# Optimization experiments

Hardware: AMD Instinct MI355X
Metric: run time of the kernel (lower is better)

Reference implementation:

```python
import jax, jax.numpy as jnp
import numpy as np
from jax import lax

# Fixed-point format: Q*.8 (8 fractional bits), as used by HGRNFixed8bit's
# to_fixed/from_fixed round-trip. We simulate it in float via round(x*256)/256.
FRAC = 256.0
EPS = 1e-5
B, T, D = 4, 2048, 2048  # batch, seq_len, hidden_size; input_dim = D (expand_ratio=1)


def to_fixed(x):
    return jnp.round(x * FRAC) / FRAC


def to_ternary(w):
    # BitNet-style ternarization: sign(w/mean|w|), zeroed where |w_norm| < 0.5
    scale = jnp.mean(jnp.abs(w))
    wn = w / (scale + 1e-5)
    t = jnp.sign(wn)
    return jnp.where(jnp.abs(wn) < 0.5, 0.0, t).astype(jnp.float32)


def per_channel_scale(w):
    # compute_scale: mean |w| over dim 0, stored in fixed point
    return to_fixed(jnp.mean(jnp.abs(w), axis=0))


def setup_inputs() -> dict:
    key = jax.random.key(0)
    ks = jax.random.split(key, 6)
    hidden_states = jax.random.normal(ks[0], (B, T, D), dtype=jnp.float32)
    # float master weights, then quantize exactly as quantize_weights() does
    w_i_f = jax.random.normal(ks[1], (D, D), dtype=jnp.float32) * 0.02  # i_proj.weight.T
    w_f_f = jax.random.normal(ks[2], (D, D), dtype=jnp.float32) * 0.02  # f_proj.weight.T
    w_g_f = jax.random.normal(ks[3], (D, D), dtype=jnp.float32) * 0.02  # g_proj.weight.T
    w_o_f = jax.random.normal(ks[4], (D, D), dtype=jnp.float32) * 0.02  # o_proj.weight [D_out, D_in]
    g_norm_w = jnp.ones((D,), dtype=jnp.float32)  # g_norm (RMSNorm-swish-gate) weight
    return {
        "hidden_states": hidden_states,
        "w_i": to_ternary(w_i_f), "w_f": to_ternary(w_f_f),
        "w_g": to_ternary(w_g_f), "w_o": to_ternary(w_o_f),
        "s_i": per_channel_scale(w_i_f), "s_f": per_channel_scale(w_f_f),
        "s_g": per_channel_scale(w_g_f), "s_o": per_channel_scale(w_o_f),
        "g_norm_w": g_norm_w,
    }


def reference(hidden_states, w_i, w_f, w_g, w_o, s_i, s_f, s_g, s_o, g_norm_w):
    # Quantize activations to 8-bit fixed point (to_fixed)
    x = to_fixed(hidden_states)                       # [B,T,D]
    # Ternary dequant-matmuls with per-channel scales
    i = jnp.einsum('btd,de->bte', x, w_i) * s_i       # input branch
    f = jax.nn.sigmoid(jnp.einsum('btd,de->bte', x, w_f) * s_f)  # forget gate
    g = jnp.einsum('btd,de->bte', x, w_g) * s_g       # output gate
    i = (1.0 - f) * i                                 # HGRN input gating
    # Gated linear recurrence h_t = f_t * h_{t-1} + i_t via associative scan
    def combine(a, b):
        af, ai = a
        bf, bi = b
        return (af * bf, ai * bf + bi)
    _, h = lax.associative_scan(combine, (f, i), axis=1)  # [B,T,E]
    # FusedRMSNormSwishGate: rmsnorm(h) * weight * swish(g)
    rms = h * lax.rsqrt(jnp.mean(h * h, axis=-1, keepdims=True) + EPS)
    o = rms * g_norm_w * (g * jax.nn.sigmoid(g))
    # Output ternary matmul (o_proj, weight untransposed -> use w_o.T),
    # per-input-channel scale, then from_fixed round-trip of the fixed output
    out = to_fixed(jnp.einsum('bte,oe->bto', o * s_o, w_o))  # [B,T,D]
    return out
```

## Files before the change

### kernel.cpp

```cpp
#include <hip/hip_runtime.h>
#include <hip/hip_bf16.h>
#include <stdint.h>
#include <math.h>


#define BATCH 4
#define SEQ   2048
#define DIM   2048
#define MROWS (BATCH*SEQ)
#define TCH   64
#define NCH   (SEQ/TCH)

#define GBM 256
#define GBN 128
#define GBK 64
#define GNT (DIM/GBK)
#define ASZ (GBM*GBK)
#define BSZ (GBN*GBK)
#define BUFSZ (ASZ+BSZ)

typedef unsigned short u16;
typedef __attribute__((ext_vector_type(8))) short short8;
typedef __attribute__((ext_vector_type(4))) float f32x4;

static __device__ __forceinline__ u16 f2bf_rne(float x) {
  uint32_t u = __float_as_uint(x);
  u += 0x7FFFu + ((u >> 16) & 1u);
  return (u16)(u >> 16);
}
static __device__ __forceinline__ float bf2f(u16 h) {
  return __uint_as_float(((uint32_t)h) << 16);
}

static __device__ __forceinline__ void gl2lds16(const void* g, void* l) {
  __builtin_amdgcn_global_load_lds((const __attribute__((address_space(1))) void*)g,
                                   (__attribute__((address_space(3))) void*)l,
                                   16, 0, 0);
}

__global__ __launch_bounds__(256) void diag_ws(float* __restrict__ out, float val) {
  size_t i = ((size_t)blockIdx.x * 256 + threadIdx.x) * 8;
#pragma unroll
  for (int j = 0; j < 8; j++) out[i + j] = val;
}

__global__ __launch_bounds__(256) void prep_x(const float* __restrict__ x,
                                              u16* __restrict__ XB) {
  size_t i = ((size_t)blockIdx.x * 256 + threadIdx.x) * 4;
  float4 v = *(const float4*)(x + i);
  float q[4] = {v.x, v.y, v.z, v.w};
  u16 hh[4];
#pragma unroll
  for (int j = 0; j < 4; j++) {
    float xq = rintf(q[j] * 256.0f) * 0.00390625f;
    hh[j] = f2bf_rne(xq);
  }
  *(uint2*)(XB + i) = make_uint2((uint32_t)hh[0] | ((uint32_t)hh[1] << 16),
                                 (uint32_t)hh[2] | ((uint32_t)hh[3] << 16));
}

__global__ void prep_wT(const float* __restrict__ w_i, const float* __restrict__ w_f,
                        const float* __restrict__ w_g, u16* __restrict__ WT) {
  __shared__ u16 tile[32][33];
  const int g = blockIdx.z;
  const float* __restrict__ w = (g == 0) ? w_i : (g == 1) ? w_f : w_g;
  u16* __restrict__ outp = WT + (size_t)g * DIM * DIM;
  const int d0 = blockIdx.x * 32;
  const int e0 = blockIdx.y * 32;
  const int tx = threadIdx.x;
  const int ty = threadIdx.y;
  for (int ii = ty; ii < 32; ii += 8)
    tile[ii][tx] = f2bf_rne(w[(size_t)(d0 + ii) * DIM + e0 + tx]);
  __syncthreads();
  for (int ii = ty; ii < 32; ii += 8)
    outp[(size_t)(e0 + ii) * DIM + d0 + tx] = tile[tx][ii];
}

__global__ __launch_bounds__(256) void prep_wo(const float* __restrict__ w, u16* __restrict__ WB) {
  size_t i = ((size_t)blockIdx.x * 256 + threadIdx.x) * 4;
  float4 v = *(const float4*)(w + i);
  *(uint2*)(WB + i) = make_uint2((uint32_t)f2bf_rne(v.x) | ((uint32_t)f2bf_rne(v.y) << 16),
                                 (uint32_t)f2bf_rne(v.z) | ((uint32_t)f2bf_rne(v.w) << 16));
}

static __device__ __forceinline__ void stage_A(const u16* ga, u16* buf, int tid) {
#pragma unroll
  for (int j = 0; j < 4; j++)
    gl2lds16(ga + (size_t)j * (64 * DIM), buf + (size_t)(tid + j * 512) * 8);
}
static __device__ __forceinline__ void stage_B(const u16* gb, u16* buf, int tid) {
#pragma unroll
  for (int j = 0; j < 2; j++)
    gl2lds16(gb + (size_t)j * (64 * DIM), buf + ASZ + (size_t)(tid + j * 512) * 8);
}

static __device__ __forceinline__ void kloop(const u16* __restrict__ Ag,
                                             const u16* __restrict__ Bg,
                                             u16* lds, f32x4 (&acc)[4][4]) {
  const int tid = threadIdx.x;
  const int lane16 = tid & 15;
  const int quad = (tid & 63) >> 4;
  const int wid = tid >> 6;
  const int waveM = wid >> 1;
  const int waveN = wid & 1;
  const int rowA = tid >> 3;
  const int cc8 = ((tid & 7) ^ (rowA & 7)) * 8;
  const u16* ga = Ag + (size_t)rowA * DIM + cc8;
  const u16* gb = Bg + (size_t)rowA * DIM + cc8;
  const int colx = (lane16 & 7) * 8;
  const int arow = (waveM * 64 + lane16) * GBK;
  const int brow = (waveN * 64 + lane16) * GBK;

  stage_A(ga, lds, tid);
  stage_B(gb, lds, tid);
  stage_A(ga + GBK, lds + BUFSZ, tid);
  stage_B(gb + GBK, lds + BUFSZ, tid);
  asm volatile("s_waitcnt vmcnt(6)" ::: "memory");
  __builtin_amdgcn_s_barrier();

  int sl = 0, st = 2;
#pragma unroll 1
  for (int t = 0; t < GNT; ++t) {
    const u16* A = lds + sl * BUFSZ;
    const u16* B = A + ASZ;
    u16* SB = lds + st * BUFSZ;
    const bool pf = (t + 2 < GNT);
    {
      short8 af[4], bf[4];
      const int c0 = (quad * 8) ^ colx;
#pragma unroll
      for (int mi = 0; mi < 4; mi++)
        af[mi] = *(const short8*)(A + arow + mi * (16 * GBK) + c0);
#pragma unroll
      for (int ni = 0; ni < 4; ni++)
        bf[ni] = *(const short8*)(B + brow + ni * (16 * GBK) + c0);
      if (pf) stage_A(ga + (size_t)(t + 2) * GBK, SB, tid);
      __builtin_amdgcn_s_barrier();
      __builtin_amdgcn_s_setprio(1);
#pragma unroll
      for (int mi = 0; mi < 4; mi++)
#pragma unroll
        for (int ni = 0; ni < 4; ni++)
          acc[mi][ni] = __builtin_amdgcn_mfma_f32_16x16x32_bf16(af[mi], bf[ni], acc[mi][ni], 0, 0, 0);
      __builtin_amdgcn_s_setprio(0);
      __builtin_amdgcn_s_barrier();
    }
    {
      short8 af[4], bf[4];
      const int c1 = (32 + quad * 8) ^ colx;
#pragma unroll
      for (int mi = 0; mi < 4; mi++)
        af[mi] = *(const short8*)(A + arow + mi * (16 * GBK) + c1);
#pragma unroll
      for (int ni = 0; ni < 4; ni++)
        bf[ni] = *(const short8*)(B + brow + ni * (16 * GBK) + c1);
      if (pf) stage_B(gb + (size_t)(t + 2) * GBK, SB, tid);
      __builtin_amdgcn_s_barrier();
      __builtin_amdgcn_s_setprio(1);
#pragma unroll
      for (int mi = 0; mi < 4; mi++)
#pragma unroll
        for (int ni = 0; ni < 4; ni++)
          acc[mi][ni] = __builtin_amdgcn_mfma_f32_16x16x32_bf16(af[mi], bf[ni], acc[mi][ni], 0, 0, 0);
      __builtin_amdgcn_s_setprio(0);
      __builtin_amdgcn_s_barrier();
    }
    if (pf) {
      asm volatile("s_waitcnt vmcnt(6)" ::: "memory");
    } else if (t + 1 < GNT) {
      asm volatile("s_waitcnt vmcnt(0)" ::: "memory");
    }
    __builtin_amdgcn_s_barrier();
    sl = (sl == 2) ? 0 : sl + 1;
    st = (st == 2) ? 0 : st + 1;
  }
}

__global__ __launch_bounds__(512, 2) void gemm_gates8(
    const u16* __restrict__ XB, const u16* __restrict__ WT,
    const float* __restrict__ s_i, const float* __restrict__ s_f, const float* __restrict__ s_g,
    const float* __restrict__ gnw, const float* __restrict__ s_o,
    u16* __restrict__ Ib, u16* __restrict__ Fb, u16* __restrict__ Gb) {
  __shared__ __align__(16) u16 lds[3 * BUFSZ];
  const int bid = blockIdx.x;
  const int i = (bid & 7) * 192 + (bid >> 3);
  const int gate = i >> 9;
  const int r = i & 511;
  const int m0 = (r >> 4) * GBM;
  const int n0 = (r & 15) * GBN;

  const u16* Ag = XB + (size_t)m0 * DIM;
  const u16* Bg = WT + (size_t)gate * DIM * DIM + (size_t)n0 * DIM;

  f32x4 acc[4][4];
#pragma unroll
  for (int a = 0; a < 4; a++)
#pragma unroll
    for (int b = 0; b < 4; b++) acc[a][b] = {0.f, 0.f, 0.f, 0.f};

  kloop(Ag, Bg, lds, acc);

  __syncthreads();
  const int tid = threadIdx.x;
  const int lane16 = tid & 15;
  const int quad = (tid & 63) >> 4;
  const int wid = tid >> 6;
  const int waveM = wid >> 1;
  const int waveN = wid & 1;
  const float* __restrict__ sc = (gate == 0) ? s_i : (gate == 1) ? s_f : s_g;
  u16* T = lds;
#pragma unroll
  for (int ni = 0; ni < 4; ni++) {
    const int n = n0 + waveN * 64 + ni * 16 + lane16;
    const float scale = sc[n];
    const float post = (gate == 2) ? gnw[n] * s_o[n] : 0.f;
    const int tcol = waveN * 64 + ni * 16 + lane16;
#pragma unroll
    for (int mi = 0; mi < 4; mi++) {
      const int lrow = waveM * 64 + mi * 16 + quad * 4;
#pragma unroll
      for (int r2 = 0; r2 < 4; r2++) {
        float v = acc[mi][ni][r2] * scale;
        if (gate == 1) v = 1.0f / (1.0f + expf(-v));
        if (gate == 2) v = v / (1.0f + expf(-v)) * post;
        T[(lrow + r2) * 136 + tcol] = f2bf_rne(v);
      }
    }
  }
  __syncthreads();
  u16* __restrict__ Out = (gate == 0) ? Ib : (gate == 1) ? Fb : Gb;
#pragma unroll
  for (int j = 0; j < 8; j++) {
    const int id = tid + j * 512;
    const int row = id >> 4;
    const int c16 = id & 15;
    uint4 v = *(const uint4*)(T + row * 136 + c16 * 8);
    *(uint4*)(Out + (size_t)(m0 + row) * DIM + n0 + c16 * 8) = v;
  }
}

__global__ __launch_bounds__(512, 2) void gemm_out8(const u16* __restrict__ OS,
                                                    const u16* __restrict__ WOB,
                                                    float* __restrict__ out) {
  __shared__ __align__(16) u16 lds[3 * BUFSZ];
  const int bid = blockIdx.x;
  const int i = (bid & 7) * 64 + (bid >> 3);
  const int m0 = (i >> 4) * GBM;
  const int n0 = (i & 15) * GBN;

  const u16* Ag = OS + (size_t)m0 * DIM;
  const u16* Bg = WOB + (size_t)n0 * DIM;

  f32x4 acc[4][4];
#pragma unroll
  for (int a = 0; a < 4; a++)
#pragma unroll
    for (int b = 0; b < 4; b++) acc[a][b] = {0.f, 0.f, 0.f, 0.f};

  kloop(Ag, Bg, lds, acc);

  __syncthreads();
  const int tid = threadIdx.x;
  const int lane16 = tid & 15;
  const int quad = (tid & 63) >> 4;
  const int wid = tid >> 6;
  const int waveM = wid >> 1;
  const int waveN = wid & 1;
  float* T = (float*)lds;
#pragma unroll
  for (int ni = 0; ni < 4; ni++) {
    const int tcol = waveN * 64 + ni * 16 + lane16;
#pragma unroll
    for (int mi = 0; mi < 4; mi++) {
      const int lrow = waveM * 64 + mi * 16 + quad * 4;
#pragma unroll
      for (int r2 = 0; r2 < 4; r2++)
        T[(lrow + r2) * 132 + tcol] = rintf(acc[mi][ni][r2] * 256.0f) * 0.00390625f;
    }
  }
  __syncthreads();
#pragma unroll
  for (int j = 0; j < 16; j++) {
    const int id = tid + j * 512;
    const int row = id >> 5;
    const int c4 = id & 31;
    float4 v = *(const float4*)(T + row * 132 + c4 * 4);
    *(float4*)(out + (size_t)(m0 + row) * DIM + n0 + c4 * 4) = v;
  }
}

__global__ __launch_bounds__(256) void scan_phase1(const u16* __restrict__ Fb,
                                                   const u16* __restrict__ Ib,
                                                   float* __restrict__ Pc,
                                                   float* __restrict__ Sc) {
  const int e0 = (blockIdx.x * 256 + threadIdx.x) * 2;
  const int c = blockIdx.y;
  const int b = blockIdx.z;
  const size_t base = ((size_t)b * SEQ + (size_t)c * TCH) * DIM + e0;
  float P0 = 1.f, S0 = 0.f, P1 = 1.f, S1 = 0.f;
  for (int t = 0; t < TCH; t++) {
    const uint32_t fp = *(const uint32_t*)(Fb + base + (size_t)t * DIM);
    const uint32_t ip = *(const uint32_t*)(Ib + base + (size_t)t * DIM);
    const float f0 = bf2f((u16)fp), f1 = bf2f((u16)(fp >> 16));
    const float i0 = bf2f((u16)ip), i1 = bf2f((u16)(ip >> 16));
    S0 = S0 * f0 + (1.f - f0) * i0;  P0 *= f0;
    S1 = S1 * f1 + (1.f - f1) * i1;  P1 *= f1;
  }
  const size_t ci = ((size_t)b * NCH + c) * DIM + e0;
  *(float2*)(Pc + ci) = make_float2(P0, P1);
  *(float2*)(Sc + ci) = make_float2(S0, S1);
}

__global__ __launch_bounds__(256) void scan_phase2(const u16* __restrict__ Fb,
                                                   const u16* __restrict__ Ib,
                                                   const float* __restrict__ Pc,
                                                   const float* __restrict__ Sc,
                                                   u16* __restrict__ Hb) {
  const int e0 = (blockIdx.x * 256 + threadIdx.x) * 2;
  const int c = blockIdx.y;
  const int b = blockIdx.z;
  float h0 = 0.f, h1 = 0.f;
  for (int cc = 0; cc < c; cc++) {
    const size_t ci = ((size_t)b * NCH + cc) * DIM + e0;
    const float2 p = *(const float2*)(Pc + ci);
    const float2 s = *(const float2*)(Sc + ci);
    h0 = s.x + p.x * h0;
    h1 = s.y + p.y * h1;
  }
  const size_t base = ((size_t)b * SEQ + (size_t)c * TCH) * DIM + e0;
  for (int t = 0; t < TCH; t++) {
    const uint32_t fp = *(const uint32_t*)(Fb + base + (size_t)t * DIM);
    const uint32_t ip = *(const uint32_t*)(Ib + base + (size_t)t * DIM);
    const float f0 = bf2f((u16)fp), f1 = bf2f((u16)(fp >> 16));
    const float i0 = bf2f((u16)ip), i1 = bf2f((u16)(ip >> 16));
    h0 = f0 * h0 + (1.f - f0) * i0;
    h1 = f1 * h1 + (1.f - f1) * i1;
    *(uint32_t*)(Hb + base + (size_t)t * DIM) =
        (uint32_t)f2bf_rne(h0) | ((uint32_t)f2bf_rne(h1) << 16);
  }
}

__global__ __launch_bounds__(256) void rms_gate(const u16* __restrict__ Hb,
                                                const u16* __restrict__ SwGb,
                                                u16* __restrict__ OS) {
  const size_t base = (size_t)blockIdx.x * DIM;
  const int tid = threadIdx.x;
  const int e0 = tid * 8;
  uint4 hp = *(const uint4*)(Hb + base + e0);
  float hv[8];
  hv[0] = bf2f((u16)hp.x); hv[1] = bf2f((u16)(hp.x >> 16));
  hv[2] = bf2f((u16)hp.y); hv[3] = bf2f((u16)(hp.y >> 16));
  hv[4] = bf2f((u16)hp.z); hv[5] = bf2f((u16)(hp.z >> 16));
  hv[6] = bf2f((u16)hp.w); hv[7] = bf2f((u16)(hp.w >> 16));
  float ss = 0.f;
#pragma unroll
  for (int j = 0; j < 8; j++) ss += hv[j] * hv[j];
#pragma unroll
  for (int off = 32; off > 0; off >>= 1) ss += __shfl_down(ss, off, 64);
  __shared__ float red[4];
  if ((tid & 63) == 0) red[tid >> 6] = ss;
  __syncthreads();
  const float tot = red[0] + red[1] + red[2] + red[3];
  const float inv = 1.0f / sqrtf(tot * (1.0f / (float)DIM) + 1e-5f);

  uint4 gp = *(const uint4*)(SwGb + base + e0);
  float gv[8];
  gv[0] = bf2f((u16)gp.x); gv[1] = bf2f((u16)(gp.x >> 16));
  gv[2] = bf2f((u16)gp.y); gv[3] = bf2f((u16)(gp.y >> 16));
  gv[4] = bf2f((u16)gp.z); gv[5] = bf2f((u16)(gp.z >> 16));
  gv[6] = bf2f((u16)gp.w); gv[7] = bf2f((u16)(gp.w >> 16));
  u16 ov[8];
#pragma unroll
  for (int j = 0; j < 8; j++) ov[j] = f2bf_rne(hv[j] * inv * gv[j]);
  uint4 op;
  op.x = (uint32_t)ov[0] | ((uint32_t)ov[1] << 16);
  op.y = (uint32_t)ov[2] | ((uint32_t)ov[3] << 16);
  op.z = (uint32_t)ov[4] | ((uint32_t)ov[5] << 16);
  op.w = (uint32_t)ov[6] | ((uint32_t)ov[7] << 16);
  *(uint4*)(OS + base + e0) = op;
}

extern "C" void kernel_launch(void* const* d_in, const int* in_sizes, int n_in,
                              void* d_out, int out_size, void* d_ws, size_t ws_size,
                              hipStream_t stream) {
  (void)in_sizes; (void)n_in; (void)out_size;
  const float* x   = (const float*)d_in[0];
  const float* w_i = (const float*)d_in[1];
  const float* w_f = (const float*)d_in[2];
  const float* w_g = (const float*)d_in[3];
  const float* w_o = (const float*)d_in[4];
  const float* s_i = (const float*)d_in[5];
  const float* s_f = (const float*)d_in[6];
  const float* s_g = (const float*)d_in[7];
  const float* s_o = (const float*)d_in[8];
  const float* gnw = (const float*)d_in[9];
  float* out = (float*)d_out;

  const size_t MB = 1024 * 1024;
  const size_t NEED = 88 * MB;
  if (ws_size < NEED) {
    diag_ws<<<MROWS * DIM / 2048, 256, 0, stream>>>(out, (float)(ws_size / MB));
    return;
  }

  uint8_t* ws = (uint8_t*)d_ws;
  u16* XB = (u16*)(ws);
  u16* WT = (u16*)(ws + 32 * MB);
  u16* Ib = (u16*)(ws + 56 * MB);
  float* Pc = (float*)(ws + 32 * MB);
  float* Sc = (float*)(ws + 33 * MB);
  u16* WOB = (u16*)(ws + 34 * MB);
  u16* Hb  = XB;
  u16* OS  = Ib;
  u16* Gb = (u16*)d_out;
  u16* Fb = (u16*)((uint8_t*)d_out + 32 * MB);

  prep_x<<<MROWS * DIM / 1024, 256, 0, stream>>>(x, XB);
  prep_wT<<<dim3(DIM / 32, DIM / 32, 3), dim3(32, 8, 1), 0, stream>>>(w_i, w_f, w_g, WT);
  gemm_gates8<<<1536, 512, 0, stream>>>(XB, WT, s_i, s_f, s_g, gnw, s_o, Ib, Fb, Gb);
  scan_phase1<<<dim3(DIM / 512, NCH, BATCH), 256, 0, stream>>>(Fb, Ib, Pc, Sc);
  scan_phase2<<<dim3(DIM / 512, NCH, BATCH), 256, 0, stream>>>(Fb, Ib, Pc, Sc, Hb);
  prep_wo<<<DIM * DIM / 1024, 256, 0, stream>>>(w_o, WOB);
  rms_gate<<<MROWS, 256, 0, stream>>>(Hb, Gb, OS);
  gemm_out8<<<512, 512, 0, stream>>>(OS, WOB, out);
}
```

Before: 551.3 us.

## Enlarge GEMM tiles to 256x256 with double-buffered LDS and 128-row waves

```diff
diff --git a/kernel.cpp b/kernel.cpp
--- a/kernel.cpp
+++ b/kernel.cpp
@@ -12,12 +12,11 @@
 #define NCH   (SEQ/TCH)
 
 #define GBM 256
-#define GBN 128
+#define GBN 256
 #define GBK 64
 #define GNT (DIM/GBK)
 #define ASZ (GBM*GBK)
 #define BSZ (GBN*GBK)
-#define BUFSZ (ASZ+BSZ)
 
 typedef unsigned short u16;
 typedef __attribute__((ext_vector_type(8))) short short8;
@@ -83,96 +82,91 @@
                                  (uint32_t)f2bf_rne(v.z) | ((uint32_t)f2bf_rne(v.w) << 16));
 }
 
-static __device__ __forceinline__ void stage_A(const u16* ga, u16* buf, int tid) {
+static __device__ __forceinline__ void stage_tile(const u16* g, u16* buf, int tid) {
 #pragma unroll
   for (int j = 0; j < 4; j++)
-    gl2lds16(ga + (size_t)j * (64 * DIM), buf + (size_t)(tid + j * 512) * 8);
-}
-static __device__ __forceinline__ void stage_B(const u16* gb, u16* buf, int tid) {
-#pragma unroll
-  for (int j = 0; j < 2; j++)
-    gl2lds16(gb + (size_t)j * (64 * DIM), buf + ASZ + (size_t)(tid + j * 512) * 8);
-}
-
-static __device__ __forceinline__ void kloop(const u16* __restrict__ Ag,
-                                             const u16* __restrict__ Bg,
-                                             u16* lds, f32x4 (&acc)[4][4]) {
+    gl2lds16(g + (size_t)j * (64 * DIM), buf + (size_t)(tid + j * 512) * 8);
+}
+
+static __device__ __forceinline__ void kloop256(const u16* __restrict__ Ag,
+                                                const u16* __restrict__ Bg,
+                                                u16* lds, f32x4 (&acc)[8][4]) {
   const int tid = threadIdx.x;
   const int lane16 = tid & 15;
   const int quad = (tid & 63) >> 4;
   const int wid = tid >> 6;
-  const int waveM = wid >> 1;
-  const int waveN = wid & 1;
-  const int rowA = tid >> 3;
-  const int cc8 = ((tid & 7) ^ (rowA & 7)) * 8;
-  const u16* ga = Ag + (size_t)rowA * DIM + cc8;
-  const u16* gb = Bg + (size_t)rowA * DIM + cc8;
+  const int waveM = wid >> 2;
+  const int waveN = wid & 3;
+  u16* ldsA = lds;
+  u16* ldsB = lds + 2 * ASZ;
+
+  const int rowS = tid >> 3;
+  const int ccS = ((tid & 7) ^ (rowS & 7)) * 8;
+  const u16* ga = Ag + (size_t)rowS * DIM + ccS;
+  const u16* gb = Bg + (size_t)rowS * DIM + ccS;
+
   const int colx = (lane16 & 7) * 8;
-  const int arow = (waveM * 64 + lane16) * GBK;
+  const int c0 = (quad * 8) ^ colx;
+  const int c1 = (32 + quad * 8) ^ colx;
+  const int arow = (waveM * 128 + lane16) * GBK;
   const int brow = (waveN * 64 + lane16) * GBK;
 
-  stage_A(ga, lds, tid);
-  stage_B(gb, lds, tid);
-  stage_A(ga + GBK, lds + BUFSZ, tid);
-  stage_B(gb + GBK, lds + BUFSZ, tid);
-  asm volatile("s_waitcnt vmcnt(6)" ::: "memory");
+  stage_tile(ga, ldsA, tid);
+  stage_tile(gb, ldsB, tid);
+  asm volatile("s_waitcnt vmcnt(0)" ::: "memory");
   __builtin_amdgcn_s_barrier();
 
-  int sl = 0, st = 2;
 #pragma unroll 1
   for (int t = 0; t < GNT; ++t) {
-    const u16* A = lds + sl * BUFSZ;
-    const u16* B = A + ASZ;
-    u16* SB = lds + st * BUFSZ;
-    const bool pf = (t + 2 < GNT);
-    {
-      short8 af[4], bf[4];
-      const int c0 = (quad * 8) ^ colx;
-#pragma unroll
-      for (int mi = 0; mi < 4; mi++)
-        af[mi] = *(const short8*)(A + arow + mi * (16 * GBK) + c0);
-#pragma unroll
-      for (int ni = 0; ni < 4; ni++)
-        bf[ni] = *(const short8*)(B + brow + ni * (16 * GBK) + c0);
-      if (pf) stage_A(ga + (size_t)(t + 2) * GBK, SB, tid);
-      __builtin_amdgcn_s_barrier();
-      __builtin_amdgcn_s_setprio(1);
-#pragma unroll
-      for (int mi = 0; mi < 4; mi++)
-#pragma unroll
-        for (int ni = 0; ni < 4; ni++)
-          acc[mi][ni] = __builtin_amdgcn_mfma_f32_16x16x32_bf16(af[mi], bf[ni], acc[mi][ni], 0, 0, 0);
-      __builtin_amdgcn_s_setprio(0);
-      __builtin_amdgcn_s_barrier();
-    }
-    {
-      short8 af[4], bf[4];
-      const int c1 = (32 + quad * 8) ^ colx;
-#pragma unroll
-      for (int mi = 0; mi < 4; mi++)
-        af[mi] = *(const short8*)(A + arow + mi * (16 * GBK) + c1);
-#pragma unroll
-      for (int ni = 0; ni < 4; ni++)
-        bf[ni] = *(const short8*)(B + brow + ni * (16 * GBK) + c1);
-      if (pf) stage_B(gb + (size_t)(t + 2) * GBK, SB, tid);
-      __builtin_amdgcn_s_barrier();
-      __builtin_amdgcn_s_setprio(1);
-#pragma unroll
-      for (int mi = 0; mi < 4; mi++)
-#pragma unroll
-        for (int ni = 0; ni < 4; ni++)
-          acc[mi][ni] = __builtin_amdgcn_mfma_f32_16x16x32_bf16(af[mi], bf[ni], acc[mi][ni], 0, 0, 0);
-      __builtin_amdgcn_s_setprio(0);
-      __builtin_amdgcn_s_barrier();
-    }
+    const u16* A = ldsA + (t & 1) * ASZ;
+    const u16* B = ldsB + (t & 1) * BSZ;
+    u16* SA = ldsA + ((t + 1) & 1) * ASZ;
+    u16* SB = ldsB + ((t + 1) & 1) * BSZ;
+    const bool pf = (t + 1 < GNT);
+
     if (pf) {
-      asm volatile("s_waitcnt vmcnt(6)" ::: "memory");
-    } else if (t + 1 < GNT) {
-      asm volatile("s_waitcnt vmcnt(0)" ::: "memory");
-    }
+      stage_tile(ga + (size_t)(t + 1) * GBK, SA, tid);
+      stage_tile(gb + (size_t)(t + 1) * GBK, SB, tid);
+    }
+
+    short8 bfr[4][2], afr[4][2];
+#pragma unroll
+    for (int ni = 0; ni < 4; ni++) {
+      bfr[ni][0] = *(const short8*)(B + brow + ni * (16 * GBK) + c0);
+      bfr[ni][1] = *(const short8*)(B + brow + ni * (16 * GBK) + c1);
+    }
+#pragma unroll
+    for (int mi = 0; mi < 4; mi++) {
+      afr[mi][0] = *(const short8*)(A + arow + mi * (16 * GBK) + c0);
+      afr[mi][1] = *(const short8*)(A + arow + mi * (16 * GBK) + c1);
+    }
+    __builtin_amdgcn_s_setprio(1);
+#pragma unroll
+    for (int mi = 0; mi < 4; mi++)
+#pragma unroll
+      for (int ni = 0; ni < 4; ni++) {
+        acc[mi][ni] = __builtin_amdgcn_mfma_f32_16x16x32_bf16(afr[mi][0], bfr[ni][0], acc[mi][ni], 0, 0, 0);
+        acc[mi][ni] = __builtin_amdgcn_mfma_f32_16x16x32_bf16(afr[mi][1], bfr[ni][1], acc[mi][ni], 0, 0, 0);
+      }
+    __builtin_amdgcn_s_setprio(0);
+
+#pragma unroll
+    for (int mi = 0; mi < 4; mi++) {
+      afr[mi][0] = *(const short8*)(A + arow + 64 * GBK + mi * (16 * GBK) + c0);
+      afr[mi][1] = *(const short8*)(A + arow + 64 * GBK + mi * (16 * GBK) + c1);
+    }
+    __builtin_amdgcn_s_setprio(1);
+#pragma unroll
+    for (int mi = 0; mi < 4; mi++)
+#pragma unroll
+      for (int ni = 0; ni < 4; ni++) {
+        acc[4 + mi][ni] = __builtin_amdgcn_mfma_f32_16x16x32_bf16(afr[mi][0], bfr[ni][0], acc[4 + mi][ni], 0, 0, 0);
+        acc[4 + mi][ni] = __builtin_amdgcn_mfma_f32_16x16x32_bf16(afr[mi][1], bfr[ni][1], acc[4 + mi][ni], 0, 0, 0);
+      }
+    __builtin_amdgcn_s_setprio(0);
+
+    if (pf) asm volatile("s_waitcnt vmcnt(0)" ::: "memory");
     __builtin_amdgcn_s_barrier();
-    sl = (sl == 2) ? 0 : sl + 1;
-    st = (st == 2) ? 0 : st + 1;
   }
 }
 
@@ -181,111 +175,106 @@
     const float* __restrict__ s_i, const float* __restrict__ s_f, const float* __restrict__ s_g,
     const float* __restrict__ gnw, const float* __restrict__ s_o,
     u16* __restrict__ Ib, u16* __restrict__ Fb, u16* __restrict__ Gb) {
-  __shared__ __align__(16) u16 lds[3 * BUFSZ];
+  __shared__ __align__(16) u16 lds[2 * ASZ + 2 * BSZ];
   const int bid = blockIdx.x;
-  const int i = (bid & 7) * 192 + (bid >> 3);
-  const int gate = i >> 9;
-  const int r = i & 511;
-  const int m0 = (r >> 4) * GBM;
-  const int n0 = (r & 15) * GBN;
+  const int i = (bid & 7) * 96 + (bid >> 3);
+  const int gate = i >> 8;
+  const int r = i & 255;
+  const int m0 = (r & 31) * GBM;
+  const int n0 = (r >> 5) * GBN;
 
   const u16* Ag = XB + (size_t)m0 * DIM;
   const u16* Bg = WT + (size_t)gate * DIM * DIM + (size_t)n0 * DIM;
 
-  f32x4 acc[4][4];
-#pragma unroll
-  for (int a = 0; a < 4; a++)
+  f32x4 acc[8][4];
+#pragma unroll
+  for (int a = 0; a < 8; a++)
 #pragma unroll
     for (int b = 0; b < 4; b++) acc[a][b] = {0.f, 0.f, 0.f, 0.f};
 
-  kloop(Ag, Bg, lds, acc);
+  kloop256(Ag, Bg, lds, acc);
 
   __syncthreads();
   const int tid = threadIdx.x;
   const int lane16 = tid & 15;
   const int quad = (tid & 63) >> 4;
   const int wid = tid >> 6;
-  const int waveM = wid >> 1;
-  const int waveN = wid & 1;
+  const int waveM = wid >> 2;
+  const int waveN = wid & 3;
   const float* __restrict__ sc = (gate == 0) ? s_i : (gate == 1) ? s_f : s_g;
+  u16* __restrict__ Out = (gate == 0) ? Ib : (gate == 1) ? Fb : Gb;
   u16* T = lds;
-#pragma unroll
-  for (int ni = 0; ni < 4; ni++) {
-    const int n = n0 + waveN * 64 + ni * 16 + lane16;
-    const float scale = sc[n];
-    const float post = (gate == 2) ? gnw[n] * s_o[n] : 0.f;
-    const int tcol = waveN * 64 + ni * 16 + lane16;
-#pragma unroll
-    for (int mi = 0; mi < 4; mi++) {
-      const int lrow = waveM * 64 + mi * 16 + quad * 4;
-#pragma unroll
-      for (int r2 = 0; r2 < 4; r2++) {
-        float v = acc[mi][ni][r2] * scale;
-        if (gate == 1) v = 1.0f / (1.0f + expf(-v));
-        if (gate == 2) v = v / (1.0f + expf(-v)) * post;
-        T[(lrow + r2) * 136 + tcol] = f2bf_rne(v);
+#pragma unroll 1
+  for (int p = 0; p < 2; ++p) {
+    if ((waveN >> 1) == p) {
+#pragma unroll
+      for (int ni = 0; ni < 4; ni++) {
+        const int n = n0 + waveN * 64 + ni * 16 + lane16;
+        const float scale = sc[n];
+        const float post = (gate == 2) ? gnw[n] * s_o[n] : 0.f;
+        const int tcol = (waveN & 1) * 64 + ni * 16 + lane16;
+#pragma unroll
+        for (int a = 0; a < 8; a++) {
+          const int lrow = waveM * 128 + (a >> 2) * 64 + (a & 3) * 16 + quad * 4;
+#pragma unroll
+          for (int r2 = 0; r2 < 4; r2++) {
+            float v = acc[a][ni][r2] * scale;
+            if (gate == 1) v = 1.0f / (1.0f + expf(-v));
+            if (gate == 2) v = v / (1.0f + expf(-v)) * post;
+            T[(lrow + r2) * 136 + tcol] = f2bf_rne(v);
+          }
+        }
       }
     }
-  }
-  __syncthreads();
-  u16* __restrict__ Out = (gate == 0) ? Ib : (gate == 1) ? Fb : Gb;
-#pragma unroll
-  for (int j = 0; j < 8; j++) {
-    const int id = tid + j * 512;
-    const int row = id >> 4;
-    const int c16 = id & 15;
-    uint4 v = *(const uint4*)(T + row * 136 + c16 * 8);
-    *(uint4*)(Out + (size_t)(m0 + row) * DIM + n0 + c16 * 8) = v;
+    __syncthreads();
+#pragma unroll
+    for (int j = 0; j < 8; j++) {
+      const int id = tid + j * 512;
+      const int row = id >> 4;
+      const int c16 = id & 15;
+      uint4 v = *(const uint4*)(T + row * 136 + c16 * 8);
+      *(uint4*)(Out + (size_t)(m0 + row) * DIM + n0 + p * 128 + c16 * 8) = v;
+    }
+    __syncthreads();
   }
 }
 
 __global__ __launch_bounds__(512, 2) void gemm_out8(const u16* __restrict__ OS,
                                                     const u16* __restrict__ WOB,
                                                     float* __restrict__ out) {
-  __shared__ __align__(16) u16 lds[3 * BUFSZ];
+  __shared__ __align__(16) u16 lds[2 * ASZ + 2 * BSZ];
   const int bid = blockIdx.x;
-  const int i = (bid & 7) * 64 + (bid >> 3);
-  const int m0 = (i >> 4) * GBM;
-  const int n0 = (i & 15) * GBN;
+  const int i = (bid & 7) * 32 + (bid >> 3);
+  const int m0 = (i & 31) * GBM;
+  const int n0 = (i >> 5) * GBN;
 
   const u16* Ag = OS + (size_t)m0 * DIM;
   const u16* Bg = WOB + (size_t)n0 * DIM;
 
-  f32x4 acc[4][4];
-#pragma unroll
-  for (int a = 0; a < 4; a++)
+  f32x4 acc[8][4];
+#pragma unroll
+  for (int a = 0; a < 8; a++)
 #pragma unroll
     for (int b = 0; b < 4; b++) acc[a][b] = {0.f, 0.f, 0.f, 0.f};
 
-  kloop(Ag, Bg, lds, acc);
-
-  __syncthreads();
+  kloop256(Ag, Bg, lds, acc);
+
   const int tid = threadIdx.x;
   const int lane16 = tid & 15;
   const int quad = (tid & 63) >> 4;
   const int wid = tid >> 6;
-  const int waveM = wid >> 1;
-  const int waveN = wid & 1;
-  float* T = (float*)lds;
+  const int waveM = wid >> 2;
+  const int waveN = wid & 3;
 #pragma unroll
   for (int ni = 0; ni < 4; ni++) {
-    const int tcol = waveN * 64 + ni * 16 + lane16;
-#pragma unroll
-    for (int mi = 0; mi < 4; mi++) {
-      const int lrow = waveM * 64 + mi * 16 + quad * 4;
+    const int n = n0 + waveN * 64 + ni * 16 + lane16;
+#pragma unroll
+    for (int a = 0; a < 8; a++) {
+      const int mrow = m0 + waveM * 128 + (a >> 2) * 64 + (a & 3) * 16 + quad * 4;
 #pragma unroll
       for (int r2 = 0; r2 < 4; r2++)
-        T[(lrow + r2) * 132 + tcol] = rintf(acc[mi][ni][r2] * 256.0f) * 0.00390625f;
-    }
-  }
-  __syncthreads();
-#pragma unroll
-  for (int j = 0; j < 16; j++) {
-    const int id = tid + j * 512;
-    const int row = id >> 5;
-    const int c4 = id & 31;
-    float4 v = *(const float4*)(T + row * 132 + c4 * 4);
-    *(float4*)(out + (size_t)(m0 + row) * DIM + n0 + c4 * 4) = v;
+        out[(size_t)(mrow + r2) * DIM + n] = rintf(acc[a][ni][r2] * 256.0f) * 0.00390625f;
+    }
   }
 }
 
@@ -417,10 +406,10 @@
 
   prep_x<<<MROWS * DIM / 1024, 256, 0, stream>>>(x, XB);
   prep_wT<<<dim3(DIM / 32, DIM / 32, 3), dim3(32, 8, 1), 0, stream>>>(w_i, w_f, w_g, WT);
-  gemm_gates8<<<1536, 512, 0, stream>>>(XB, WT, s_i, s_f, s_g, gnw, s_o, Ib, Fb, Gb);
+  gemm_gates8<<<768, 512, 0, stream>>>(XB, WT, s_i, s_f, s_g, gnw, s_o, Ib, Fb, Gb);
   scan_phase1<<<dim3(DIM / 512, NCH, BATCH), 256, 0, stream>>>(Fb, Ib, Pc, Sc);
   scan_phase2<<<dim3(DIM / 512, NCH, BATCH), 256, 0, stream>>>(Fb, Ib, Pc, Sc, Hb);
   prep_wo<<<DIM * DIM / 1024, 256, 0, stream>>>(w_o, WOB);
   rms_gate<<<MROWS, 256, 0, stream>>>(Hb, Gb, OS);
-  gemm_out8<<<512, 512, 0, stream>>>(OS, WOB, out);
-}
+  gemm_out8<<<256, 512, 0, stream>>>(OS, WOB, out);
+}
```

Result: no change. 560.9 us (+1.7%).
